# Kernel optimization log

Hardware: AMD Instinct MI355X
Metric: run time of the kernel (lower is better)

## Reference

```python
import jax, jax.numpy as jnp
import numpy as np

B, L, D, F, T = 32, 768, 256, 256, 3072
_EPS = 1e-5


def _layernorm(h, g, b):
    mu = jnp.mean(h, axis=-1, keepdims=True)
    var = jnp.var(h, axis=-1, keepdims=True)
    return (h - mu) * jax.lax.rsqrt(var + _EPS) * g + b


def _conv1d(h, w, b):
    # h: [B, L, Cin], w: [K, Cin, Cout] (HIO), padding=1 matches torch Conv1d(padding=1)
    return jax.lax.conv_general_dilated(h, w, (1,), [(1, 1)], dimension_numbers=('NHC', 'HIO', 'NHC')) + b


def setup_inputs() -> dict:
    key = jax.random.key(0)
    ks = jax.random.split(key, 6)
    return {
        'x': jax.random.normal(ks[0], (B, L, D), jnp.float32),
        'target': jax.random.randint(ks[1], (B, L), 0, 4, jnp.int32),
        'mel_max_length': T,
        'conv1_w': jax.random.normal(ks[2], (3, D, F), jnp.float32) * 0.05,
        'conv1_b': jnp.zeros((F,), jnp.float32),
        'ln1_g': jnp.ones((F,), jnp.float32),
        'ln1_b': jnp.zeros((F,), jnp.float32),
        'conv2_w': jax.random.normal(ks[3], (3, F, F), jnp.float32) * 0.05,
        'conv2_b': jnp.zeros((F,), jnp.float32),
        'ln2_g': jnp.ones((F,), jnp.float32),
        'ln2_b': jnp.zeros((F,), jnp.float32),
        'lin_w': jax.random.normal(ks[4], (F, 1), jnp.float32) * 0.05,
        'lin_b': jnp.zeros((1,), jnp.float32),
    }


def reference(x, target, mel_max_length, conv1_w, conv1_b, ln1_g, ln1_b,
              conv2_w, conv2_b, ln2_g, ln2_b, lin_w, lin_b):
    alpha = 1.0
    # DurationPredictor: conv -> relu -> LN -> conv -> relu -> LN -> linear (dropout=0)
    h = _layernorm(jax.nn.relu(_conv1d(x, conv1_w, conv1_b)), ln1_g, ln1_b)
    h = _layernorm(jax.nn.relu(_conv1d(h, conv2_w, conv2_b)), ln2_g, ln2_b)
    dp_out = (h @ lin_w + lin_b)[..., 0]                       # [B, L]
    durations = jnp.exp(dp_out) * alpha                        # [B, L] float
    # Training branch: durations come from target
    dpo = jnp.round(target.astype(jnp.float32) * alpha).astype(jnp.int32)  # [B, L]
    # LR: alignment @ x realized as cumulative-duration searchsorted + gather
    cum = jnp.cumsum(dpo, axis=1)                              # [B, L]
    t = jnp.arange(mel_max_length, dtype=jnp.int32)            # [T]
    idx = jax.vmap(lambda c: jnp.searchsorted(c, t, side='right'))(cum)  # [B, T]
    mask = (t[None, :] < cum[:, -1:]).astype(x.dtype)          # [B, T] zero past total frames
    out = jnp.take_along_axis(x, jnp.clip(idx, 0, x.shape[1] - 1)[:, :, None], axis=1)
    out = out * mask[:, :, None]                               # [B, T, D]
    return (out, dpo, durations)
```

## Files before the change

### kernel.cpp

```cpp
#include <hip/hip_runtime.h>
#include <hip/hip_bf16.h>
#include <math.h>

#define BB 32
#define LL 768
#define DD 256
#define FF 256
#define TT 3072
#define MT 48
#define PAD 262
#define A1R 66

typedef __attribute__((ext_vector_type(8))) short bf16x8;
typedef __attribute__((ext_vector_type(4))) float f32x4;

__device__ inline unsigned short f2b(float f) {
    union { float f; unsigned u; } v; v.f = f;
    unsigned r = (v.u + 0x7FFF + ((v.u >> 16) & 1)) >> 16;
    return (unsigned short)r;
}

__device__ inline unsigned cvt_pk_bf16(float lo, float hi) {
    unsigned r;
    asm("v_cvt_pk_bf16_f32 %0, %1, %2" : "=v"(r) : "v"(lo), "v"(hi));
    return r;
}

#define DPP_ROR_ADD(v, ctrl)                                                   \
    v += __int_as_float(__builtin_amdgcn_update_dpp(                           \
        0, __float_as_int(v), ctrl, 0xF, 0xF, false))

__device__ inline void red16_pair(float& a, float& b) {
    DPP_ROR_ADD(a, 0x128); DPP_ROR_ADD(b, 0x128);
    DPP_ROR_ADD(a, 0x124); DPP_ROR_ADD(b, 0x124);
    DPP_ROR_ADD(a, 0x122); DPP_ROR_ADD(b, 0x122);
    DPP_ROR_ADD(a, 0x121); DPP_ROR_ADD(b, 0x121);
}

__device__ inline float red16_one(float a) {
    DPP_ROR_ADD(a, 0x128);
    DPP_ROR_ADD(a, 0x124);
    DPP_ROR_ADD(a, 0x122);
    DPP_ROR_ADD(a, 0x121);
    return a;
}

__global__ __launch_bounds__(256) void prep_scan_kernel(
    const float* __restrict__ w1, const float* __restrict__ w2,
    unsigned short* __restrict__ wQ1, unsigned short* __restrict__ wQ2,
    const int* __restrict__ target,
    float* __restrict__ out_dpo,
    int* __restrict__ idx_map)
{
    __shared__ int tsum[256];
    const int tid = threadIdx.x;

    if (blockIdx.x < 48) {
        const int layer = blockIdx.x / 24;
        const int s  = blockIdx.x % 24;
        const int kc = s >> 3, c8 = s & 7;
        const float* __restrict__ w = layer ? w2 : w1;
        unsigned short* __restrict__ o = (layer ? wQ2 : wQ1) + s * 8192 + tid * 32;
        const int n = tid;

        alignas(16) unsigned short tmp[32];
#pragma unroll
        for (int q = 0; q < 4; ++q)
#pragma unroll
            for (int j = 0; j < 8; ++j) {
                const int cin = c8 * 32 + q * 8 + j;
                tmp[q * 8 + j] = f2b(w[((size_t)(kc * 256 + cin)) * 256 + n]);
            }
#pragma unroll
        for (int i = 0; i < 4; ++i)
            *reinterpret_cast<uint4*>(o + i * 8) = *reinterpret_cast<const uint4*>(tmp + i * 8);
        return;
    }

    const int b = blockIdx.x - 48;

    const int l = 3 * tid;
    const int v0 = target[b * LL + l];
    const int v1 = target[b * LL + l + 1];
    const int v2 = target[b * LL + l + 2];
    out_dpo[b * LL + l]     = (float)v0;
    out_dpo[b * LL + l + 1] = (float)v1;
    out_dpo[b * LL + l + 2] = (float)v2;

    const int s0 = v0, s1 = v0 + v1, s2 = v0 + v1 + v2;
    tsum[tid] = s2;
    __syncthreads();
    for (int off = 1; off < 256; off <<= 1) {
        int xq = (tid >= off) ? tsum[tid - off] : 0;
        __syncthreads();
        tsum[tid] += xq;
        __syncthreads();
    }
    const int excl = tsum[tid] - s2;

    for (int t = tid; t < TT; t += 256) idx_map[b * TT + t] = -1;
    __syncthreads();

    const int c0 = excl + s0, c1 = excl + s1, c2 = excl + s2;
    for (int t = excl; t < c0 && t < TT; ++t) idx_map[b * TT + t] = l;
    for (int t = c0;   t < c1 && t < TT; ++t) idx_map[b * TT + t] = l + 1;
    for (int t = c1;   t < c2 && t < TT; ++t) idx_map[b * TT + t] = l + 2;
}

__global__ __launch_bounds__(256, 2) void fused_dp_kernel(
    const float* __restrict__ x,
    const unsigned short* __restrict__ wQ1,
    const unsigned short* __restrict__ wQ2,
    const float* __restrict__ c1b, const float* __restrict__ g1, const float* __restrict__ b1,
    const float* __restrict__ c2b, const float* __restrict__ g2, const float* __restrict__ b2,
    const float* __restrict__ lw,  const float* __restrict__ lb,
    float* __restrict__ out_dur)
{
    __shared__ union {
        unsigned short A1[A1R * PAD];
        unsigned short h2[50 * PAD];
    } sm;
    __shared__ float red[4][4][4][4][2];
    __shared__ float redp[4][3][4][4];
    __shared__ float fin[50][2];

    const int tid  = threadIdx.x;
    const int b    = blockIdx.x / (LL / MT);
    const int l0   = (blockIdx.x % (LL / MT)) * MT;
    const int wave = tid >> 6, lane = tid & 63;
    const int quad = lane >> 4, l16 = lane & 15;

    int   cols[4];
    float c1bv[4], g1v[4], b1v[4], c2bv[4], g2v[4], b2v[4], lwv[4];
#pragma unroll
    for (int nt = 0; nt < 4; ++nt) {
        const int c = wave * 64 + nt * 16 + l16;
        cols[nt] = c;
        c1bv[nt] = c1b[c]; g1v[nt] = g1[c]; b1v[nt] = b1[c];
        c2bv[nt] = c2b[c]; g2v[nt] = g2[c]; b2v[nt] = b2[c];
        lwv[nt]  = lw[c];
    }
    const float lbv = lb[0];

    {
        float4 v0[7], v1[7];
        int lr[7];
#pragma unroll
        for (int k = 0; k < 7; ++k) {
            const int q  = tid + (k << 8);
            const int ar = q >> 5;
            const int l  = l0 - 2 + ar;
            lr[k] = (ar < 52 && l >= 0 && l < LL) ? l : -1;
            if (lr[k] >= 0) {
                const float* pp = x + ((size_t)b * LL + lr[k]) * DD + (q & 31) * 8;
                v0[k] = *reinterpret_cast<const float4*>(pp);
                v1[k] = *reinterpret_cast<const float4*>(pp + 4);
            }
        }
#pragma unroll
        for (int k = 0; k < 7; ++k) {
            const int q  = tid + (k << 8);
            const int ar = q >> 5;
            uint4 uu = {0u, 0u, 0u, 0u};
            if (lr[k] >= 0) {
                uu.x = cvt_pk_bf16(v0[k].x, v0[k].y);
                uu.y = cvt_pk_bf16(v0[k].z, v0[k].w);
                uu.z = cvt_pk_bf16(v1[k].x, v1[k].y);
                uu.w = cvt_pk_bf16(v1[k].z, v1[k].w);
            }
            *reinterpret_cast<uint4*>(&sm.A1[ar * PAD + (q & 31) * 8]) = uu;
        }
        for (int q = tid; q < 320; q += 256) {
            const int ar = 56 + (q >> 5);
            uint4 z = {0u, 0u, 0u, 0u};
            *reinterpret_cast<uint4*>(&sm.A1[ar * PAD + (q & 31) * 8]) = z;
        }
    }

    f32x4 acc1[4][4] = {};
    {
        bf16x8 br[4][4], ar2[2][4];
        auto ldb1 = [&](int buf, int s) {
#pragma unroll
            for (int nt = 0; nt < 4; ++nt)
                br[buf][nt] = *reinterpret_cast<const bf16x8*>(
                    wQ1 + (size_t)s * 8192 + cols[nt] * 32 + quad * 8);
        };
        auto lda1 = [&](int buf, int s) {
            const int kc = s >> 3, c8 = s & 7;
#pragma unroll
            for (int mt = 0; mt < 4; ++mt)
                ar2[buf][mt] = *reinterpret_cast<const bf16x8*>(
                    &sm.A1[(16 * mt + l16 + kc) * PAD + c8 * 32 + quad * 8]);
        };
        auto mm1 = [&](int ab, int bb) {
            __builtin_amdgcn_s_setprio(1);
#pragma unroll
            for (int mt = 0; mt < 4; ++mt)
#pragma unroll
                for (int nt = 0; nt < 4; ++nt)
                    acc1[mt][nt] = __builtin_amdgcn_mfma_f32_16x16x32_bf16(
                        ar2[ab][mt], br[bb][nt], acc1[mt][nt], 0, 0, 0);
            __builtin_amdgcn_s_setprio(0);
        };
        ldb1(0, 0);
        ldb1(1, 1);
        __syncthreads();
        lda1(0, 0);
#pragma unroll
        for (int s = 0; s < 24; ++s) {
            if (s + 2 < 24) ldb1((s + 2) & 3, s + 2);
            if (s + 1 < 24) lda1((s + 1) & 1, s + 1);
            mm1(s & 1, s & 3);
        }
    }
    __syncthreads();

#pragma unroll
    for (int mt = 0; mt < 4; ++mt)
#pragma unroll
        for (int r = 0; r < 4; ++r) {
            float s1 = 0.f, s2 = 0.f;
#pragma unroll
            for (int nt = 0; nt < 4; ++nt) {
                const float v = fmaxf(acc1[mt][nt][r] + c1bv[nt], 0.f);
                s1 += v; s2 += v * v;
            }
            red16_pair(s1, s2);
            if (l16 == 0) { red[wave][mt][quad][r][0] = s1; red[wave][mt][quad][r][1] = s2; }
        }
    __syncthreads();
    if (tid < 50) {
        const int mt = tid >> 4, q = (tid >> 2) & 3, r = tid & 3;
        const float s1 = red[0][mt][q][r][0] + red[1][mt][q][r][0]
                       + red[2][mt][q][r][0] + red[3][mt][q][r][0];
        const float s2 = red[0][mt][q][r][1] + red[1][mt][q][r][1]
                       + red[2][mt][q][r][1] + red[3][mt][q][r][1];
        const float mu  = s1 * (1.f / 256.f);
        const float var = s2 * (1.f / 256.f) - mu * mu;
        fin[tid][0] = mu;
        fin[tid][1] = rsqrtf(var + 1e-5f);
    }
    __syncthreads();

#pragma unroll
    for (int mt = 0; mt < 4; ++mt)
#pragma unroll
        for (int r = 0; r < 4; ++r) {
            const int rho = 16 * mt + quad * 4 + r;
            if (rho < 50) {
                const int gr = l0 - 1 + rho;
                const float mu = fin[rho][0], rstd = fin[rho][1];
#pragma unroll
                for (int nt = 0; nt < 4; ++nt) {
                    unsigned short hv = 0;
                    if (gr >= 0 && gr < LL) {
                        const float v = fmaxf(acc1[mt][nt][r] + c1bv[nt], 0.f);
                        hv = f2b((v - mu) * rstd * g1v[nt] + b1v[nt]);
                    }
                    sm.h2[rho * PAD + cols[nt]] = hv;
                }
            }
        }

    f32x4 acc2[3][4] = {};
    {
        bf16x8 br[4][4], ar2[2][3];
        auto ldb2 = [&](int buf, int s) {
#pragma unroll
            for (int nt = 0; nt < 4; ++nt)
                br[buf][nt] = *reinterpret_cast<const bf16x8*>(
                    wQ2 + (size_t)s * 8192 + cols[nt] * 32 + quad * 8);
        };
        auto lda2 = [&](int buf, int s) {
            const int kc = s >> 3, c8 = s & 7;
#pragma unroll
            for (int mt = 0; mt < 3; ++mt)
                ar2[buf][mt] = *reinterpret_cast<const bf16x8*>(
                    &sm.h2[(16 * mt + l16 + kc) * PAD + c8 * 32 + quad * 8]);
        };
        auto mm2 = [&](int ab, int bb) {
            __builtin_amdgcn_s_setprio(1);
#pragma unroll
            for (int mt = 0; mt < 3; ++mt)
#pragma unroll
                for (int nt = 0; nt < 4; ++nt)
                    acc2[mt][nt] = __builtin_amdgcn_mfma_f32_16x16x32_bf16(
                        ar2[ab][mt], br[bb][nt], acc2[mt][nt], 0, 0, 0);
            __builtin_amdgcn_s_setprio(0);
        };
        ldb2(0, 0);
        ldb2(1, 1);
        __syncthreads();
        lda2(0, 0);
#pragma unroll
        for (int s = 0; s < 24; ++s) {
            if (s + 2 < 24) ldb2((s + 2) & 3, s + 2);
            if (s + 1 < 24) lda2((s + 1) & 1, s + 1);
            mm2(s & 1, s & 3);
        }
    }

#pragma unroll
    for (int mt = 0; mt < 3; ++mt)
#pragma unroll
        for (int r = 0; r < 4; ++r) {
            float s1 = 0.f, s2 = 0.f;
#pragma unroll
            for (int nt = 0; nt < 4; ++nt) {
                const float v = fmaxf(acc2[mt][nt][r] + c2bv[nt], 0.f);
                s1 += v; s2 += v * v;
            }
            red16_pair(s1, s2);
            if (l16 == 0) { red[wave][mt][quad][r][0] = s1; red[wave][mt][quad][r][1] = s2; }
        }
    __syncthreads();
    if (tid < MT) {
        const int mt = tid >> 4, q = (tid >> 2) & 3, r = tid & 3;
        const float s1 = red[0][mt][q][r][0] + red[1][mt][q][r][0]
                       + red[2][mt][q][r][0] + red[3][mt][q][r][0];
        const float s2 = red[0][mt][q][r][1] + red[1][mt][q][r][1]
                       + red[2][mt][q][r][1] + red[3][mt][q][r][1];
        const float mu  = s1 * (1.f / 256.f);
        const float var = s2 * (1.f / 256.f) - mu * mu;
        fin[tid][0] = mu;
        fin[tid][1] = rsqrtf(var + 1e-5f);
    }
    __syncthreads();

#pragma unroll
    for (int mt = 0; mt < 3; ++mt)
#pragma unroll
        for (int r = 0; r < 4; ++r) {
            const int rho = 16 * mt + quad * 4 + r;
            const float mu = fin[rho][0], rstd = fin[rho][1];
            float p = 0.f;
#pragma unroll
            for (int nt = 0; nt < 4; ++nt) {
                const float v = fmaxf(acc2[mt][nt][r] + c2bv[nt], 0.f);
                p += ((v - mu) * rstd * g2v[nt] + b2v[nt]) * lwv[nt];
            }
            p = red16_one(p);
            if (l16 == 0) redp[wave][mt][quad][r] = p;
        }
    __syncthreads();
    if (tid < MT) {
        const int mt = tid >> 4, q = (tid >> 2) & 3, r = tid & 3;
        const float dp = redp[0][mt][q][r] + redp[1][mt][q][r]
                       + redp[2][mt][q][r] + redp[3][mt][q][r] + lbv;
        out_dur[(size_t)b * LL + l0 + tid] = expf(dp);
    }
}

__global__ __launch_bounds__(256) void gather_kernel(
    const float* __restrict__ x,
    const int* __restrict__ idx_map,
    float* __restrict__ out)
{
    const int wv = threadIdx.x >> 6, lane = threadIdx.x & 63;
    const int row = blockIdx.x * 4 + wv;
    const int b = row / TT, t = row - b * TT;
    const int idx = idx_map[b * TT + t];
    f32x4 val = {0.f, 0.f, 0.f, 0.f};
    if (idx >= 0)
        val = *reinterpret_cast<const f32x4*>(x + ((size_t)(b * LL + idx)) * DD + lane * 4);
    __builtin_nontemporal_store(val, reinterpret_cast<f32x4*>(out) + (size_t)row * (DD / 4) + lane);
}

extern "C" void kernel_launch(void* const* d_in, const int* in_sizes, int n_in,
                              void* d_out, int out_size, void* d_ws, size_t ws_size,
                              hipStream_t stream)
{
    const float* x      = (const float*)d_in[0];
    const int*   target = (const int*)  d_in[1];
    const float* c1w = (const float*)d_in[3];
    const float* c1b = (const float*)d_in[4];
    const float* g1  = (const float*)d_in[5];
    const float* b1  = (const float*)d_in[6];
    const float* c2w = (const float*)d_in[7];
    const float* c2b = (const float*)d_in[8];
    const float* g2  = (const float*)d_in[9];
    const float* b2  = (const float*)d_in[10];
    const float* lw  = (const float*)d_in[11];
    const float* lb  = (const float*)d_in[12];

    float* out0    = (float*)d_out;
    float* out_dpo = out0 + (size_t)BB * TT * DD;
    float* out_dur = out_dpo + (size_t)BB * LL;

    char* ws = (char*)d_ws;
    unsigned short* wQ1 = (unsigned short*)ws;                 ws += (size_t)24 * 8192 * 2;
    unsigned short* wQ2 = (unsigned short*)ws;                 ws += (size_t)24 * 8192 * 2;
    int* idx_map        = (int*)ws;

    prep_scan_kernel<<<48 + BB, 256, 0, stream>>>(
        c1w, c2w, wQ1, wQ2, target, out_dpo, idx_map);

    fused_dp_kernel<<<BB * (LL / MT), 256, 0, stream>>>(
        x, wQ1, wQ2, c1b, g1, b1, c2b, g2, b2, lw, lb, out_dur);

    gather_kernel<<<BB * TT / 4, 256, 0, stream>>>(x, idx_map, out0);
}
```

Baseline: 193.4 us.

## Fold final LayerNorm+linear into one reduction pass and use wave-shuffle scan

```diff
diff --git a/kernel.cpp b/kernel.cpp
--- a/kernel.cpp
+++ b/kernel.cpp
@@ -37,12 +37,11 @@
     DPP_ROR_ADD(a, 0x121); DPP_ROR_ADD(b, 0x121);
 }
 
-__device__ inline float red16_one(float a) {
-    DPP_ROR_ADD(a, 0x128);
-    DPP_ROR_ADD(a, 0x124);
-    DPP_ROR_ADD(a, 0x122);
-    DPP_ROR_ADD(a, 0x121);
-    return a;
+__device__ inline void red16_tri(float& a, float& b, float& c) {
+    DPP_ROR_ADD(a, 0x128); DPP_ROR_ADD(b, 0x128); DPP_ROR_ADD(c, 0x128);
+    DPP_ROR_ADD(a, 0x124); DPP_ROR_ADD(b, 0x124); DPP_ROR_ADD(c, 0x124);
+    DPP_ROR_ADD(a, 0x122); DPP_ROR_ADD(b, 0x122); DPP_ROR_ADD(c, 0x122);
+    DPP_ROR_ADD(a, 0x121); DPP_ROR_ADD(b, 0x121); DPP_ROR_ADD(c, 0x121);
 }
 
 __global__ __launch_bounds__(256) void prep_scan_kernel(
@@ -52,7 +51,7 @@
     float* __restrict__ out_dpo,
     int* __restrict__ idx_map)
 {
-    __shared__ int tsum[256];
+    __shared__ int wsum[4];
     const int tid = threadIdx.x;
 
     if (blockIdx.x < 48) {
@@ -77,7 +76,8 @@
         return;
     }
 
-    const int b = blockIdx.x - 48;
+    const int b  = blockIdx.x - 48;
+    const int wv = tid >> 6, lane = tid & 63;
 
     const int l = 3 * tid;
     const int v0 = target[b * LL + l];
@@ -88,18 +88,22 @@
     out_dpo[b * LL + l + 2] = (float)v2;
 
     const int s0 = v0, s1 = v0 + v1, s2 = v0 + v1 + v2;
-    tsum[tid] = s2;
-    __syncthreads();
-    for (int off = 1; off < 256; off <<= 1) {
-        int xq = (tid >= off) ? tsum[tid - off] : 0;
-        __syncthreads();
-        tsum[tid] += xq;
-        __syncthreads();
-    }
-    const int excl = tsum[tid] - s2;
+
+    int inc = s2;
+#pragma unroll
+    for (int off = 1; off < 64; off <<= 1) {
+        const int t = __shfl_up(inc, off, 64);
+        if (lane >= off) inc += t;
+    }
+    if (lane == 63) wsum[wv] = inc;
 
     for (int t = tid; t < TT; t += 256) idx_map[b * TT + t] = -1;
     __syncthreads();
+
+    int woff = 0;
+#pragma unroll
+    for (int w = 0; w < 4; ++w) woff += (w < wv) ? wsum[w] : 0;
+    const int excl = woff + inc - s2;
 
     const int c0 = excl + s0, c1 = excl + s1, c2 = excl + s2;
     for (int t = excl; t < c0 && t < TT; ++t) idx_map[b * TT + t] = l;
@@ -120,9 +124,9 @@
         unsigned short A1[A1R * PAD];
         unsigned short h2[50 * PAD];
     } sm;
-    __shared__ float red[4][4][4][4][2];
-    __shared__ float redp[4][3][4][4];
+    __shared__ float red[4][4][4][4][3];
     __shared__ float fin[50][2];
+    __shared__ float cst[4][2];
 
     const int tid  = threadIdx.x;
     const int b    = blockIdx.x / (LL / MT);
@@ -141,6 +145,17 @@
         lwv[nt]  = lw[c];
     }
     const float lbv = lb[0];
+
+    {
+        float sgl = 0.f, sbl = 0.f;
+#pragma unroll
+        for (int nt = 0; nt < 4; ++nt) {
+            sgl += g2v[nt] * lwv[nt];
+            sbl += b2v[nt] * lwv[nt];
+        }
+        red16_pair(sgl, sbl);
+        if (lane == 0) { cst[wave][0] = sgl; cst[wave][1] = sbl; }
+    }
 
     {
         float4 v0[7], v1[7];
@@ -214,7 +229,6 @@
             mm1(s & 1, s & 3);
         }
     }
-    __syncthreads();
 
 #pragma unroll
     for (int mt = 0; mt < 4; ++mt)
@@ -305,49 +319,36 @@
     for (int mt = 0; mt < 3; ++mt)
 #pragma unroll
         for (int r = 0; r < 4; ++r) {
-            float s1 = 0.f, s2 = 0.f;
+            float s1 = 0.f, s2 = 0.f, svgl = 0.f;
 #pragma unroll
             for (int nt = 0; nt < 4; ++nt) {
                 const float v = fmaxf(acc2[mt][nt][r] + c2bv[nt], 0.f);
-                s1 += v; s2 += v * v;
-            }
-            red16_pair(s1, s2);
-            if (l16 == 0) { red[wave][mt][quad][r][0] = s1; red[wave][mt][quad][r][1] = s2; }
+                s1 += v; s2 += v * v; svgl += v * g2v[nt] * lwv[nt];
+            }
+            red16_tri(s1, s2, svgl);
+            if (l16 == 0) {
+                red[wave][mt][quad][r][0] = s1;
+                red[wave][mt][quad][r][1] = s2;
+                red[wave][mt][quad][r][2] = svgl;
+            }
         }
     __syncthreads();
+
     if (tid < MT) {
         const int mt = tid >> 4, q = (tid >> 2) & 3, r = tid & 3;
-        const float s1 = red[0][mt][q][r][0] + red[1][mt][q][r][0]
-                       + red[2][mt][q][r][0] + red[3][mt][q][r][0];
-        const float s2 = red[0][mt][q][r][1] + red[1][mt][q][r][1]
-                       + red[2][mt][q][r][1] + red[3][mt][q][r][1];
-        const float mu  = s1 * (1.f / 256.f);
-        const float var = s2 * (1.f / 256.f) - mu * mu;
-        fin[tid][0] = mu;
-        fin[tid][1] = rsqrtf(var + 1e-5f);
-    }
-    __syncthreads();
-
-#pragma unroll
-    for (int mt = 0; mt < 3; ++mt)
-#pragma unroll
-        for (int r = 0; r < 4; ++r) {
-            const int rho = 16 * mt + quad * 4 + r;
-            const float mu = fin[rho][0], rstd = fin[rho][1];
-            float p = 0.f;
-#pragma unroll
-            for (int nt = 0; nt < 4; ++nt) {
-                const float v = fmaxf(acc2[mt][nt][r] + c2bv[nt], 0.f);
-                p += ((v - mu) * rstd * g2v[nt] + b2v[nt]) * lwv[nt];
-            }
-            p = red16_one(p);
-            if (l16 == 0) redp[wave][mt][quad][r] = p;
-        }
-    __syncthreads();
-    if (tid < MT) {
-        const int mt = tid >> 4, q = (tid >> 2) & 3, r = tid & 3;
-        const float dp = redp[0][mt][q][r] + redp[1][mt][q][r]
-                       + redp[2][mt][q][r] + redp[3][mt][q][r] + lbv;
+        float s1 = 0.f, s2 = 0.f, svgl = 0.f, SGL = 0.f, SBL = 0.f;
+#pragma unroll
+        for (int w = 0; w < 4; ++w) {
+            s1   += red[w][mt][q][r][0];
+            s2   += red[w][mt][q][r][1];
+            svgl += red[w][mt][q][r][2];
+            SGL  += cst[w][0];
+            SBL  += cst[w][1];
+        }
+        const float mu   = s1 * (1.f / 256.f);
+        const float var  = s2 * (1.f / 256.f) - mu * mu;
+        const float rstd = rsqrtf(var + 1e-5f);
+        const float dp   = rstd * (svgl - mu * SGL) + SBL + lbv;
         out_dur[(size_t)b * LL + l0 + tid] = expf(dp);
     }
 }
```

After: 193.2 us. Within noise of the previous version (-0.1%).
